# Optimization experiments

Hardware: AMD Instinct MI355X
Metric: run time of the kernel (lower is better)

## Reference

```python
import jax, jax.numpy as jnp
import numpy as np

B, T, E, H, NH, L, R, K, N, P, HOR = 32, 16, 768, 1024, 16, 6, 8, 16, 100000, 9, 8
HD = H // NH


def _ln(x, g, b):
    m = jnp.mean(x, -1, keepdims=True)
    v = jnp.mean((x - m) ** 2, -1, keepdims=True)
    return (x - m) * jax.lax.rsqrt(v + 1e-5) * g + b


def _lora(x, W, A, Bm, b):
    # base linear + low-rank update: x W^T + (x A^T) B^T + b
    return x @ W.T + (x @ A.T) @ Bm.T + b


def setup_inputs() -> dict:
    key = jax.random.key(0)
    ks = iter(jax.random.split(key, 64))
    def rn(shape, s):
        return jax.random.normal(next(ks), shape, dtype=jnp.float32) * s
    d = {}
    d['history_img_emb'] = rn((B, T, E), 1.0)
    d['current_emb'] = rn((B, E), 1.0)
    d['goal_emb'] = rn((B, E), 1.0)
    d['subgoal_emb'] = rn((B, E), 1.0)
    d['beacon_emb'] = rn((B, E), 1.0)
    d['history_proprio'] = rn((B, T, P), 1.0)
    d['proprio'] = rn((B, P), 1.0)
    d['bank'] = rn((N, E), 1.0)
    d['hp_W'] = rn((H, E + P), 0.02); d['hp_b'] = jnp.zeros((H,), jnp.float32)
    d['ip_W'] = rn((H, E), 0.02); d['ip_b'] = jnp.zeros((H,), jnp.float32)
    d['pp_W'] = rn((H, P), 0.02); d['pp_b'] = jnp.zeros((H,), jnp.float32)
    d['plan_token'] = rn((1, 1, H), 0.02)
    d['ln1_g'] = jnp.ones((L, H), jnp.float32); d['ln1_b'] = jnp.zeros((L, H), jnp.float32)
    d['ln2_g'] = jnp.ones((L, H), jnp.float32); d['ln2_b'] = jnp.zeros((L, H), jnp.float32)
    for nm, o, i in (('q', H, H), ('k', H, H), ('v', H, H), ('o', H, H), ('f1', 4 * H, H), ('f2', H, 4 * H)):
        d[nm + 'W'] = rn((L, o, i), 0.02)
        d[nm + 'A'] = rn((L, R, i), 0.02)
        d[nm + 'B'] = rn((L, o, R), 0.02)
        d[nm + 'b'] = jnp.zeros((L, o), jnp.float32)
    d['fln_g'] = jnp.ones((H,), jnp.float32); d['fln_b'] = jnp.zeros((H,), jnp.float32)
    d['ah_W1'] = rn((H, H), 0.02); d['ah_b1'] = jnp.zeros((H,), jnp.float32)
    d['ah_W2'] = rn((3, H), 0.02); d['ah_b2'] = jnp.zeros((3,), jnp.float32)
    d['rh_W1'] = rn((H, H + 3), 0.02); d['rh_b1'] = jnp.zeros((H,), jnp.float32)
    d['rh_W2'] = rn((HOR * 3, H), 0.02); d['rh_b2'] = jnp.zeros((HOR * 3,), jnp.float32)
    d['sh_W'] = rn((1, H), 0.02); d['sh_b'] = jnp.zeros((1,), jnp.float32)
    return d


def reference(history_img_emb, current_emb, goal_emb, subgoal_emb, beacon_emb,
              history_proprio, proprio, bank,
              hp_W, hp_b, ip_W, ip_b, pp_W, pp_b, plan_token,
              ln1_g, ln1_b, ln2_g, ln2_b,
              qW, qA, qB, qb, kW, kA, kB, kb, vW, vA, vB, vb, oW, oA, oB, ob,
              f1W, f1A, f1B, f1b, f2W, f2A, f2B, f2b,
              fln_g, fln_b, ah_W1, ah_b1, ah_W2, ah_b2,
              rh_W1, rh_b1, rh_W2, rh_b2, sh_W, sh_b):
    # batched semantic-bank top-k retrieval (replaces the per-sample python loop)
    sims = current_emb @ bank.T                      # [B, N]
    scores, idx = jax.lax.top_k(sims, K)             # [B, K]
    sem = bank[idx] * scores[..., None]              # [B, K, E] gather + scale

    # multi-modal token fusion
    hist = jnp.concatenate([history_img_emb, history_proprio], -1) @ hp_W.T + hp_b  # [B, T, H]
    img = lambda e: e @ ip_W.T + ip_b
    goal_t = img(goal_emb)[:, None]
    sub_t = img(subgoal_emb)[:, None]
    bea_t = img(beacon_emb)[:, None]
    sem_t = img(sem)                                 # [B, K, H]
    prop_t = (proprio @ pp_W.T + pp_b)[:, None]
    plan_t = jnp.broadcast_to(plan_token, (B, 1, H))
    x = jnp.concatenate([plan_t, hist, goal_t, sub_t, bea_t, sem_t, prop_t], 1)  # [B, S=37, H]

    scale = 1.0 / np.sqrt(HD).astype(np.float32)
    for l in range(L):
        h = _ln(x, ln1_g[l], ln1_b[l])
        q = _lora(h, qW[l], qA[l], qB[l], qb[l]).reshape(B, -1, NH, HD)
        k = _lora(h, kW[l], kA[l], kB[l], kb[l]).reshape(B, -1, NH, HD)
        v = _lora(h, vW[l], vA[l], vB[l], vb[l]).reshape(B, -1, NH, HD)
        attn = jax.nn.softmax(jnp.einsum('bshd,bthd->bhst', q, k) * scale, axis=-1)
        out = jnp.einsum('bhst,bthd->bshd', attn, v).reshape(B, -1, H)
        x = x + _lora(out, oW[l], oA[l], oB[l], ob[l])
        h2 = _ln(x, ln2_g[l], ln2_b[l])
        x = x + _lora(jax.nn.gelu(_lora(h2, f1W[l], f1A[l], f1B[l], f1b[l]), approximate=False),
                      f2W[l], f2A[l], f2B[l], f2b[l])

    x = _ln(x, fln_g, fln_b)
    ps = x[:, 0]                                     # plan token state [B, H]
    anchor = jax.nn.gelu(ps @ ah_W1.T + ah_b1, approximate=False) @ ah_W2.T + ah_b2  # [B, 3]
    ref_in = jnp.concatenate([ps, anchor], -1)
    waypoints = (jax.nn.gelu(ref_in @ rh_W1.T + rh_b1, approximate=False) @ rh_W2.T + rh_b2).reshape(B, HOR, 3)
    stop_logit = (ps @ sh_W.T + sh_b)[:, 0]          # [B]
    return anchor, waypoints, stop_logit
```

## Files before the change

### kernel.cpp

```cpp
#include <hip/hip_runtime.h>
#include <float.h>
#include <math.h>

#define NB 100000
#define SEQ 37
#define NTOK 1184
#define TKCH 16

typedef __attribute__((ext_vector_type(8))) short short8;
typedef __attribute__((ext_vector_type(4))) float floatx4;

__device__ __forceinline__ short f2bf(float f) {
  union { float f; unsigned u; } x; x.f = f;
  unsigned r = x.u + 0x7fff + ((x.u >> 16) & 1);
  return (short)(r >> 16);
}

__device__ __forceinline__ float gelu_f(float v) {
  return 0.5f * v * (1.f + erff(v * 0.70710678118654752f));
}

__global__ __launch_bounds__(256) void wconv_all(const float* __restrict__ qW,
                                                 const float* __restrict__ kW,
                                                 const float* __restrict__ vW,
                                                 const float* __restrict__ oW,
                                                 const float* __restrict__ f1W,
                                                 const float* __restrict__ f2W,
                                                 short* __restrict__ wb) {
  const int l = blockIdx.x / 1536;
  const int t = blockIdx.x - l * 1536;
  const float* src; int Kd; size_t doff; int np, kc;
  if (t < 512) {
    const int w = t >> 7, ti = t & 127;
    const float* base = (w == 0) ? qW : (w == 1) ? kW : (w == 2) ? vW : oW;
    src = base + (size_t)l * 1024 * 1024;
    Kd = 1024; np = ti >> 4; kc = ti & 15;
    doff = (size_t)w * 1048576 + ((size_t)np * 16 + kc) * 8192;
  } else if (t < 1024) {
    const int ti = t - 512;
    src = f1W + (size_t)l * 4096 * 1024;
    Kd = 1024; np = ti >> 4; kc = ti & 15;
    doff = (size_t)4 * 1048576 + ((size_t)np * 16 + kc) * 8192;
  } else {
    const int ti = t - 1024;
    src = f2W + (size_t)l * 1024 * 4096;
    Kd = 4096; np = ti >> 6; kc = ti & 63;
    doff = (size_t)8 * 1048576 + ((size_t)np * 64 + kc) * 8192;
  }
  short* dst = wb + (size_t)l * 12 * 1048576 + doff;
  const float* sp = src + (size_t)(np * 128) * Kd + kc * 64;
  const int tid = threadIdx.x;
#pragma unroll
  for (int q = 0; q < 4; ++q) {
    const int d = q * 256 + tid;
    const int row = d >> 3, slot = d & 7;
    const int ss = slot ^ (row & 7);
    const float* s = sp + (size_t)row * Kd + ss * 8;
    const float4 u0 = *(const float4*)s;
    const float4 u1 = *(const float4*)(s + 4);
    short8 v;
    v[0] = f2bf(u0.x); v[1] = f2bf(u0.y); v[2] = f2bf(u0.z); v[3] = f2bf(u0.w);
    v[4] = f2bf(u1.x); v[5] = f2bf(u1.y); v[6] = f2bf(u1.z); v[7] = f2bf(u1.w);
    *(short8*)(dst + (size_t)d * 8) = v;
  }
}

__global__ __launch_bounds__(256) void gemm_bt(const float* __restrict__ A, int lda,
                                               const short* __restrict__ WT, size_t wzstride,
                                               const float* __restrict__ b0,
                                               const float* __restrict__ b1,
                                               const float* __restrict__ b2,
                                               const float* __restrict__ LT,
                                               const float* __restrict__ B0,
                                               const float* __restrict__ B1,
                                               const float* __restrict__ B2,
                                               float* __restrict__ C, size_t czstride,
                                               int ldc, int M, int K,
                                               int acc_flag, int gelu_flag,
                                               int ksn, float* __restrict__ part) {
  __shared__ short Al[2][64 * 64];
  __shared__ short Wl[2][128 * 64];
  const int z = blockIdx.z;
  const int kidx = (ksn > 1) ? z : 0;
  const float* bias = (ksn > 1 || z == 0) ? b0 : (z == 1) ? b1 : b2;
  const float* Bz = (ksn > 1 || z == 0) ? B0 : (z == 1) ? B1 : B2;
  if (ksn == 1) C += (size_t)z * czstride;
  const int nkc_tot = K >> 6;
  const int nkc = nkc_tot / ksn;
  const short* wt = WT + (size_t)((ksn > 1) ? 0 : z) * wzstride +
                    ((size_t)blockIdx.y * nkc_tot + (size_t)kidx * nkc) * 8192;
  const int tid = threadIdx.x;
  const int wid = tid >> 6, lane = tid & 63;
  const int wr = wid >> 1, wc = wid & 1;
  const int bm = blockIdx.x * 64, bn = blockIdx.y * 128;
  const int arow = tid >> 2;
  const int s0 = (tid & 3) * 2;

  floatx4 acc[2][4];
#pragma unroll
  for (int i = 0; i < 2; ++i)
#pragma unroll
    for (int j = 0; j < 4; ++j)
#pragma unroll
      for (int r = 0; r < 4; ++r) acc[i][j][r] = 0.f;

  const int ga = bm + arow;
  const bool aok = ga < M;
  const float* ap = A + (size_t)ga * lda + (size_t)kidx * nkc * 64;
  const int aswz = arow & 7;

  float4 ar[4];
  short8 wreg[4];

#define LOAD_A(kc_)                                                        \
  {                                                                        \
    _Pragma("unroll") for (int j = 0; j < 2; ++j) {                        \
      const int slot = s0 + j;                                             \
      if (aok) {                                                           \
        ar[j * 2] = *(const float4*)(ap + (kc_)*64 + slot * 8);            \
        ar[j * 2 + 1] = *(const float4*)(ap + (kc_)*64 + slot * 8 + 4);    \
      } else {                                                             \
        ar[j * 2] = make_float4(0.f, 0.f, 0.f, 0.f);                      \
        ar[j * 2 + 1] = make_float4(0.f, 0.f, 0.f, 0.f);                  \
      }                                                                    \
    }                                                                      \
  }
#define LOAD_W(kc_)                                                        \
  {                                                                        \
    _Pragma("unroll") for (int it = 0; it < 4; ++it)                       \
        wreg[it] = *(const short8*)(wt + (size_t)(kc_)*8192 + (it * 256 + tid) * 8); \
  }
#define WRITE_A(buf_)                                                      \
  {                                                                        \
    _Pragma("unroll") for (int j = 0; j < 2; ++j) {                        \
      const int slot = s0 + j;                                             \
      short8 s;                                                            \
      s[0] = f2bf(ar[j * 2].x); s[1] = f2bf(ar[j * 2].y);                  \
      s[2] = f2bf(ar[j * 2].z); s[3] = f2bf(ar[j * 2].w);                  \
      s[4] = f2bf(ar[j * 2 + 1].x); s[5] = f2bf(ar[j * 2 + 1].y);          \
      s[6] = f2bf(ar[j * 2 + 1].z); s[7] = f2bf(ar[j * 2 + 1].w);          \
      *(short8*)&Al[buf_][arow * 64 + ((slot ^ aswz) << 3)] = s;           \
    }                                                                      \
  }
#define WRITE_W(buf_)                                                      \
  {                                                                        \
    _Pragma("unroll") for (int it = 0; it < 4; ++it)                       \
        *(short8*)&Wl[buf_][(it * 256 + tid) * 8] = wreg[it];              \
  }

  LOAD_W(0) LOAD_A(0)
  WRITE_A(0) WRITE_W(0)
  __syncthreads();

  for (int t = 0; t < nkc; ++t) {
    const int cur = t & 1, nxt = cur ^ 1;
    const bool more = (t + 1 < nkc);
    if (more) { LOAD_W(t + 1) LOAD_A(t + 1) }
#pragma unroll
    for (int ks = 0; ks < 2; ++ks) {
      short8 af[2], wf[4];
#pragma unroll
      for (int i = 0; i < 2; ++i) {
        const int row = wr * 32 + i * 16 + (lane & 15);
        const int sa = (ks * 4 + (lane >> 4)) ^ (row & 7);
        af[i] = *(const short8*)&Al[cur][row * 64 + sa * 8];
      }
#pragma unroll
      for (int j = 0; j < 4; ++j) {
        const int col = wc * 64 + j * 16 + (lane & 15);
        const int sw2 = (ks * 4 + (lane >> 4)) ^ (col & 7);
        wf[j] = *(const short8*)&Wl[cur][col * 64 + sw2 * 8];
      }
#pragma unroll
      for (int i = 0; i < 2; ++i)
#pragma unroll
        for (int j = 0; j < 4; ++j)
          acc[i][j] = __builtin_amdgcn_mfma_f32_16x16x32_bf16(af[i], wf[j], acc[i][j], 0, 0, 0);
    }
    if (more) { WRITE_A(nxt) WRITE_W(nxt) }
    __syncthreads();
  }
#undef LOAD_A
#undef LOAD_W
#undef WRITE_A
#undef WRITE_W

  if (ksn > 1) {
#pragma unroll
    for (int i = 0; i < 2; ++i) {
      const int gm0 = bm + wr * 32 + i * 16 + (lane >> 4) * 4;
#pragma unroll
      for (int r = 0; r < 4; ++r) {
        const int gm = gm0 + r;
        if (gm >= M) continue;
#pragma unroll
        for (int j = 0; j < 4; ++j) {
          const int gn = bn + wc * 64 + j * 16 + (lane & 15);
          part[((size_t)kidx * M + gm) * ldc + gn] = acc[i][j][r];
        }
      }
    }
    return;
  }

  float br[4][8];
  if (LT) {
#pragma unroll
    for (int j = 0; j < 4; ++j) {
      const int gn = bn + wc * 64 + j * 16 + (lane & 15);
      const float4 u0 = *(const float4*)(Bz + (size_t)gn * 8);
      const float4 u1 = *(const float4*)(Bz + (size_t)gn * 8 + 4);
      br[j][0] = u0.x; br[j][1] = u0.y; br[j][2] = u0.z; br[j][3] = u0.w;
      br[j][4] = u1.x; br[j][5] = u1.y; br[j][6] = u1.z; br[j][7] = u1.w;
    }
  }
#pragma unroll
  for (int i = 0; i < 2; ++i) {
    const int gm0 = bm + wr * 32 + i * 16 + (lane >> 4) * 4;
#pragma unroll
    for (int r = 0; r < 4; ++r) {
      const int gm = gm0 + r;
      if (gm >= M) continue;
      float lt[8];
      if (LT) {
        const float4 t0 = *(const float4*)(LT + ((size_t)z * NTOK + gm) * 8);
        const float4 t1 = *(const float4*)(LT + ((size_t)z * NTOK + gm) * 8 + 4);
        lt[0] = t0.x; lt[1] = t0.y; lt[2] = t0.z; lt[3] = t0.w;
        lt[4] = t1.x; lt[5] = t1.y; lt[6] = t1.z; lt[7] = t1.w;
      }
#pragma unroll
      for (int j = 0; j < 4; ++j) {
        const int gn = bn + wc * 64 + j * 16 + (lane & 15);
        float o = acc[i][j][r] + bias[gn];
        if (LT)
          o += lt[0] * br[j][0] + lt[1] * br[j][1] + lt[2] * br[j][2] + lt[3] * br[j][3] +
               lt[4] * br[j][4] + lt[5] * br[j][5] + lt[6] * br[j][6] + lt[7] * br[j][7];
        const size_t off = (size_t)gm * ldc + gn;
        if (acc_flag) o += C[off];
        if (gelu_flag) o = gelu_f(o);
        C[off] = o;
      }
    }
  }
}

__global__ __launch_bounds__(256) void reduce_f2(const float* __restrict__ part,
                                                 const float* __restrict__ bias,
                                                 const float* __restrict__ LT,
                                                 const float* __restrict__ Bm,
                                                 float* __restrict__ X) {
  const int idx = blockIdx.x * 256 + threadIdx.x;
  if (idx >= NTOK * 1024) return;
  const int gm = idx >> 10, gn = idx & 1023;
  float s = part[idx] + part[(size_t)NTOK * 1024 + idx] +
            part[(size_t)2 * NTOK * 1024 + idx] + part[(size_t)3 * NTOK * 1024 + idx];
  const float* t = LT + (size_t)gm * 8;
  const float* bp = Bm + (size_t)gn * 8;
  s += t[0] * bp[0] + t[1] * bp[1] + t[2] * bp[2] + t[3] * bp[3] +
       t[4] * bp[4] + t[5] * bp[5] + t[6] * bp[6] + t[7] * bp[7];
  X[idx] += s + bias[gn];
}

__global__ __launch_bounds__(256) void gemm_bf16(const float* __restrict__ A, int lda,
                                                 const float* __restrict__ W, int ldw,
                                                 const float* __restrict__ bias,
                                                 float* __restrict__ C,
                                                 int ldc, int M, int N, int K, int acc_flag) {
  __shared__ short Al[128 * 64];
  __shared__ short Wl[128 * 64];
  const int tid = threadIdx.x;
  const int wid = tid >> 6, lane = tid & 63;
  const int wr = wid >> 1, wc = wid & 1;
  const int bm = blockIdx.x * 128, bn = blockIdx.y * 128;
  const int srow = tid >> 1;
  const int sbase = (tid & 1) * 4;

  floatx4 acc[4][4];
#pragma unroll
  for (int i = 0; i < 4; ++i)
#pragma unroll
    for (int j = 0; j < 4; ++j)
#pragma unroll
      for (int r = 0; r < 4; ++r) acc[i][j][r] = 0.f;

  const int ga = bm + srow;
  const int gw = bn + srow;
  const bool aok = ga < M;
  const float* ap = A + (size_t)ga * lda;
  const float* wp = W + (size_t)gw * ldw;
  const int aswz = (srow & 7);
  const int dsbase = srow * 64;

  for (int kc = 0; kc < K; kc += 64) {
    __syncthreads();
    const bool kfull = (kc + 64 <= K);
    {
      const bool fast = aok && kfull && ((lda & 3) == 0);
#pragma unroll
      for (int j = 0; j < 4; ++j) {
        const int slot = sbase + j, k0 = slot * 8;
        float v[8];
        if (fast) {
          float4 u0 = *(const float4*)(ap + kc + k0);
          float4 u1 = *(const float4*)(ap + kc + k0 + 4);
          v[0] = u0.x; v[1] = u0.y; v[2] = u0.z; v[3] = u0.w;
          v[4] = u1.x; v[5] = u1.y; v[6] = u1.z; v[7] = u1.w;
        } else {
#pragma unroll
          for (int e = 0; e < 8; ++e) {
            int kk = kc + k0 + e;
            v[e] = (aok && kk < K) ? ap[kk] : 0.f;
          }
        }
        short8 s;
#pragma unroll
        for (int e = 0; e < 8; ++e) s[e] = f2bf(v[e]);
        *(short8*)&Al[dsbase + ((slot ^ aswz) << 3)] = s;
      }
    }
    {
      const bool fast = kfull && ((ldw & 3) == 0);
#pragma unroll
      for (int j = 0; j < 4; ++j) {
        const int slot = sbase + j, k0 = slot * 8;
        float v[8];
        if (fast) {
          float4 u0 = *(const float4*)(wp + kc + k0);
          float4 u1 = *(const float4*)(wp + kc + k0 + 4);
          v[0] = u0.x; v[1] = u0.y; v[2] = u0.z; v[3] = u0.w;
          v[4] = u1.x; v[5] = u1.y; v[6] = u1.z; v[7] = u1.w;
        } else {
#pragma unroll
          for (int e = 0; e < 8; ++e) {
            int kk = kc + k0 + e;
            v[e] = (kk < K) ? wp[kk] : 0.f;
          }
        }
        short8 s;
#pragma unroll
        for (int e = 0; e < 8; ++e) s[e] = f2bf(v[e]);
        *(short8*)&Wl[dsbase + ((slot ^ aswz) << 3)] = s;
      }
    }
    __syncthreads();
#pragma unroll
    for (int ks = 0; ks < 2; ++ks) {
      short8 af[4], wf[4];
#pragma unroll
      for (int i = 0; i < 4; ++i) {
        const int row = wr * 64 + i * 16 + (lane & 15);
        const int sa = (ks * 4 + (lane >> 4)) ^ (row & 7);
        af[i] = *(const short8*)&Al[row * 64 + sa * 8];
        const int col = wc * 64 + i * 16 + (lane & 15);
        const int sw = (ks * 4 + (lane >> 4)) ^ (col & 7);
        wf[i] = *(const short8*)&Wl[col * 64 + sw * 8];
      }
#pragma unroll
      for (int i = 0; i < 4; ++i)
#pragma unroll
        for (int j = 0; j < 4; ++j)
          acc[i][j] = __builtin_amdgcn_mfma_f32_16x16x32_bf16(af[i], wf[j], acc[i][j], 0, 0, 0);
    }
  }
#pragma unroll
  for (int i = 0; i < 4; ++i) {
    const int gm0 = bm + wr * 64 + i * 16 + (lane >> 4) * 4;
#pragma unroll
    for (int j = 0; j < 4; ++j) {
      const int gn = bn + wc * 64 + j * 16 + (lane & 15);
#pragma unroll
      for (int r = 0; r < 4; ++r) {
        const int gm = gm0 + r;
        if (gm < M) {
          float o = acc[i][j][r] + bias[gn];
          size_t off = (size_t)gm * ldc + gn;
          if (acc_flag) o += C[off];
          C[off] = o;
        }
      }
    }
  }
}

__global__ __launch_bounds__(256) void gemm_sm2(const float* __restrict__ A, int lda,
                                                const float* __restrict__ W, int ldw,
                                                const float* __restrict__ bias,
                                                float* __restrict__ C, int ldc,
                                                float* __restrict__ part,
                                                int N, int K, int gelu_flag) {
  __shared__ float buf[8192];
  const int tid = threadIdx.x;
  const int col = tid >> 3, ksub = tid & 7;
  const int gcol = blockIdx.x * 32 + col;
  const int KS = gridDim.y, ky = blockIdx.y;
  const int kchunk = (((K + KS - 1) / KS) + 127) & ~127;
  const int kstart = ky * kchunk;
  const int kend = (kstart + kchunk < K) ? (kstart + kchunk) : K;
  const float* wp = W + (size_t)(gcol < N ? gcol : 0) * ldw;

  float acc[32];
#pragma unroll
  for (int m = 0; m < 32; ++m) acc[m] = 0.f;

  for (int kc = kstart; kc < kend; kc += 128) {
    __syncthreads();
#pragma unroll
    for (int q = 0; q < 4; ++q) {
      const int idx4 = q * 256 + tid;
      const int m = idx4 >> 5, j = (idx4 & 31) * 4;
      const int gk = kc + j;
      float4 v;
      if (gk + 3 < K) {
        v = *(const float4*)(A + (size_t)m * lda + gk);
      } else {
        v.x = (gk < K) ? A[(size_t)m * lda + gk] : 0.f;
        v.y = (gk + 1 < K) ? A[(size_t)m * lda + gk + 1] : 0.f;
        v.z = (gk + 2 < K) ? A[(size_t)m * lda + gk + 2] : 0.f;
        v.w = (gk + 3 < K) ? A[(size_t)m * lda + gk + 3] : 0.f;
      }
      *(float4*)&buf[m * 128 + j] = v;
    }
    __syncthreads();
#pragma unroll
    for (int kk = 0; kk < 4; ++kk) {
      const int j = kk * 32 + ksub * 4;
      const int gk = kc + j;
      float4 w4 = make_float4(0.f, 0.f, 0.f, 0.f);
      if (gcol < N && gk < K) {
        if (gk + 3 < K) {
          w4 = *(const float4*)(wp + gk);
        } else {
          w4.x = wp[gk];
          if (gk + 1 < K) w4.y = wp[gk + 1];
          if (gk + 2 < K) w4.z = wp[gk + 2];
        }
      }
#pragma unroll
      for (int m = 0; m < 32; ++m) {
        const float4 a4 = *(const float4*)&buf[m * 128 + j];
        acc[m] += a4.x * w4.x + a4.y * w4.y + a4.z * w4.z + a4.w * w4.w;
      }
    }
  }
  __syncthreads();
#pragma unroll
  for (int m = 0; m < 32; ++m) buf[m * 256 + ksub * 32 + col] = acc[m];
  __syncthreads();
#pragma unroll
  for (int g = 0; g < 4; ++g) {
    const int idx = g * 256 + tid;
    const int m = idx >> 5, c = idx & 31;
    float s = 0.f;
#pragma unroll
    for (int h = 0; h < 8; ++h) s += buf[m * 256 + h * 32 + c];
    const int gc = blockIdx.x * 32 + c;
    if (gc < N) {
      if (KS == 1) {
        float o = s + bias[gc];
        if (gelu_flag) o = gelu_f(o);
        C[(size_t)m * ldc + gc] = o;
      } else {
        part[((size_t)ky * 32 + m) * N + gc] = s;
      }
    }
  }
}

__global__ __launch_bounds__(256) void reduce_sm(const float* __restrict__ part,
                                                 const float* __restrict__ bias,
                                                 float* __restrict__ C, int ldc,
                                                 int N, int KS, int gelu_flag) {
  const int idx = blockIdx.x * 256 + threadIdx.x;
  if (idx >= 32 * N) return;
  const int m = idx / N, c = idx - m * N;
  float s = 0.f;
  for (int h = 0; h < KS; ++h) s += part[((size_t)h * 32 + m) * N + c];
  float o = s + bias[c];
  if (gelu_flag) o = gelu_f(o);
  C[(size_t)m * ldc + c] = o;
}

__global__ __launch_bounds__(256) void sims_kernel(const float* __restrict__ cur,
                                                   const float* __restrict__ bank,
                                                   float* __restrict__ sims) {
  __shared__ float Bs[32][132];
  __shared__ float Cs[32][36];
  const int tid = threadIdx.x;
  const int tx = tid & 7;
  const int ty = tid >> 3;
  const int n0 = blockIdx.x * 128;
  const int srow = tid >> 1;
  const int spart = tid & 1;
  const int cb = tid >> 3;
  const int ck = (tid & 7) * 4;

  float acc[4][4] = {{0.f,0.f,0.f,0.f},{0.f,0.f,0.f,0.f},
                     {0.f,0.f,0.f,0.f},{0.f,0.f,0.f,0.f}};

  const bool rok = (n0 + srow) < NB;
  const float* bp = bank + (size_t)(n0 + srow) * 768 + spart * 16;
  const float* cp = cur + (size_t)cb * 768 + ck;

  for (int kc = 0; kc < 768; kc += 32) {
    __syncthreads();
#pragma unroll
    for (int jj = 0; jj < 4; ++jj) {
      float4 v = rok ? *(const float4*)(bp + kc + jj * 4)
                     : make_float4(0.f, 0.f, 0.f, 0.f);
      const int kk = spart * 16 + jj * 4;
      Bs[kk + 0][srow] = v.x; Bs[kk + 1][srow] = v.y;
      Bs[kk + 2][srow] = v.z; Bs[kk + 3][srow] = v.w;
    }
    {
      float4 v = *(const float4*)(cp + kc);
      Cs[ck + 0][cb] = v.x; Cs[ck + 1][cb] = v.y;
      Cs[ck + 2][cb] = v.z; Cs[ck + 3][cb] = v.w;
    }
    __syncthreads();
#pragma unroll
    for (int kk = 0; kk < 32; ++kk) {
      float4 av = *(const float4*)&Bs[kk][ty * 4];
      float4 bv = *(const float4*)&Cs[kk][tx * 4];
      float a4[4] = {av.x, av.y, av.z, av.w};
      float b4[4] = {bv.x, bv.y, bv.z, bv.w};
#pragma unroll
      for (int i = 0; i < 4; ++i)
#pragma unroll
        for (int j = 0; j < 4; ++j) acc[i][j] += a4[i] * b4[j];
    }
  }
  const int n = n0 + ty * 4;
#pragma unroll
  for (int j = 0; j < 4; ++j) {
    const int b = tx * 4 + j;
    float4 o = make_float4(acc[0][j], acc[1][j], acc[2][j], acc[3][j]);
    if (n + 3 < NB) {
      *(float4*)(sims + (size_t)b * NB + n) = o;
    } else {
      float oo[4] = {o.x, o.y, o.z, o.w};
      for (int i = 0; i < 4; ++i)
        if (n + i < NB) sims[(size_t)b * NB + n + i] = oo[i];
    }
  }
}

__global__ __launch_bounds__(256) void topk_stage1(const float* __restrict__ sims,
                                                   float* __restrict__ cv,
                                                   int* __restrict__ ci) {
  __shared__ float ss[4096];
  __shared__ int si[4096];
  __shared__ float wv[4];
  __shared__ int wi[4];
  const int chunk = blockIdx.x, b = blockIdx.y, tid = threadIdx.x;
  const int start = chunk * (NB / TKCH), end = start + (NB / TKCH);
  float ls[16]; int li[16];
#pragma unroll
  for (int i = 0; i < 16; ++i) { ls[i] = -FLT_MAX; li[i] = 0x7fffffff; }
  const float* row = sims + (size_t)b * NB;
  float lmin = -FLT_MAX;
  for (int n = start + tid; n < end; n += 256) {
    float v = row[n];
    if (v > lmin) {
      int p = 15;
      while (p > 0 && ls[p - 1] < v) { ls[p] = ls[p - 1]; li[p] = li[p - 1]; --p; }
      ls[p] = v; li[p] = n;
      lmin = ls[15];
    }
  }
#pragma unroll
  for (int i = 0; i < 16; ++i) { ss[i * 256 + tid] = ls[i]; si[i * 256 + tid] = li[i]; }
  __syncthreads();
  for (int round = 0; round < 16; ++round) {
    float bv = -FLT_MAX; int bi = 0x7fffffff;
#pragma unroll
    for (int i = 0; i < 16; ++i) {
      float v = ss[i * 256 + tid]; int ix = si[i * 256 + tid];
      if (v > bv || (v == bv && ix < bi)) { bv = v; bi = ix; }
    }
#pragma unroll
    for (int s = 32; s; s >>= 1) {
      float ov = __shfl_down(bv, s); int oi = __shfl_down(bi, s);
      if (ov > bv || (ov == bv && oi < bi)) { bv = ov; bi = oi; }
    }
    if ((tid & 63) == 0) { wv[tid >> 6] = bv; wi[tid >> 6] = bi; }
    __syncthreads();
    if (tid == 0) {
      bv = wv[0]; bi = wi[0];
      for (int w = 1; w < 4; ++w)
        if (wv[w] > bv || (wv[w] == bv && wi[w] < bi)) { bv = wv[w]; bi = wi[w]; }
      cv[(b * TKCH + chunk) * 16 + round] = bv;
      ci[(b * TKCH + chunk) * 16 + round] = bi;
      wi[0] = bi;
    }
    __syncthreads();
    bi = wi[0];
#pragma unroll
    for (int i = 0; i < 16; ++i)
      if (si[i * 256 + tid] == bi) ss[i * 256 + tid] = -FLT_MAX;
    __syncthreads();
  }
}

__global__ __launch_bounds__(256) void topk_stage2(const float* __restrict__ cv,
                                                   const int* __restrict__ ci,
                                                   float* __restrict__ tks,
                                                   int* __restrict__ tki) {
  __shared__ float wv[4];
  __shared__ int wi[4];
  __shared__ int bw;
  const int b = blockIdx.x, tid = threadIdx.x;
  float val = cv[b * 256 + tid];
  int idx = ci[b * 256 + tid];
  for (int round = 0; round < 16; ++round) {
    float bv = val; int bi = idx;
#pragma unroll
    for (int s = 1; s < 64; s <<= 1) {
      float ov = __shfl_xor(bv, s); int oi = __shfl_xor(bi, s);
      if (ov > bv || (ov == bv && oi < bi)) { bv = ov; bi = oi; }
    }
    if ((tid & 63) == 0) { wv[tid >> 6] = bv; wi[tid >> 6] = bi; }
    __syncthreads();
    if (tid == 0) {
      bv = wv[0]; bi = wi[0];
      for (int w = 1; w < 4; ++w)
        if (wv[w] > bv || (wv[w] == bv && wi[w] < bi)) { bv = wv[w]; bi = wi[w]; }
      tks[b * 16 + round] = bv; tki[b * 16 + round] = bi;
      bw = bi;
    }
    __syncthreads();
    if (idx == bw) val = -FLT_MAX;
  }
}

__global__ void sem_kernel(const float* __restrict__ bank, const float* __restrict__ tks,
                           const int* __restrict__ tki, float* __restrict__ sem) {
  int slot = blockIdx.x;
  float s = tks[slot]; int idx = tki[slot];
  for (int i = threadIdx.x; i < 768; i += 256)
    sem[(size_t)slot * 768 + i] = bank[(size_t)idx * 768 + i] * s;
}

__global__ void build_hist_in(const float* __restrict__ img, const float* __restrict__ pr,
                              float* __restrict__ out) {
  int r = blockIdx.x;
  for (int i = threadIdx.x; i < 777; i += 256)
    out[(size_t)r * 777 + i] = (i < 768) ? img[(size_t)r * 768 + i] : pr[r * 9 + (i - 768)];
}

__global__ void build_img_in(const float* __restrict__ goal, const float* __restrict__ sub,
                             const float* __restrict__ bea, const float* __restrict__ sem,
                             float* __restrict__ out) {
  int r = blockIdx.x;
  const float* src = (r < 32) ? goal + (size_t)r * 768
                   : (r < 64) ? sub + (size_t)(r - 32) * 768
                   : (r < 96) ? bea + (size_t)(r - 64) * 768
                              : sem + (size_t)(r - 96) * 768;
  for (int i = threadIdx.x; i < 768; i += 256) out[(size_t)r * 768 + i] = src[i];
}

__global__ void assemble_x(const float* __restrict__ th, const float* __restrict__ ti,
                           const float* __restrict__ tp, const float* __restrict__ plan,
                           float* __restrict__ x) {
  int r = blockIdx.x;
  int b = r / SEQ, tok = r - b * SEQ;
  const float* src;
  if (tok == 0) src = plan;
  else if (tok <= 16) src = th + (size_t)(b * 16 + tok - 1) * 1024;
  else if (tok <= 19) src = ti + (size_t)((tok - 17) * 32 + b) * 1024;
  else if (tok <= 35) src = ti + (size_t)(96 + b * 16 + (tok - 20)) * 1024;
  else src = tp + (size_t)b * 1024;
  for (int i = threadIdx.x; i < 1024; i += 256) x[(size_t)r * 1024 + i] = src[i];
}

__global__ void build_ref(const float* __restrict__ ps, const float* __restrict__ anc,
                          float* __restrict__ ref) {
  int b = blockIdx.x;
  for (int i = threadIdx.x; i < 1027; i += 256)
    ref[(size_t)b * 1027 + i] = (i < 1024) ? ps[(size_t)b * 1024 + i] : anc[b * 3 + (i - 1024)];
}

__device__ __forceinline__ float block_sum256(float v, float* red) {
#pragma unroll
  for (int s = 32; s; s >>= 1) v += __shfl_down(v, s);
  if ((threadIdx.x & 63) == 0) red[threadIdx.x >> 6] = v;
  __syncthreads();
  float tot = red[0] + red[1] + red[2] + red[3];
  __syncthreads();
  return tot;
}

__global__ __launch_bounds__(256) void ln_kernel(const float* __restrict__ in, int in_stride,
                                                 float* __restrict__ out,
                                                 const float* __restrict__ g,
                                                 const float* __restrict__ bt) {
  __shared__ float red[4];
  const float* xr = in + (size_t)blockIdx.x * in_stride;
  const int tid = threadIdx.x;
  float v[4];
#pragma unroll
  for (int i = 0; i < 4; ++i) v[i] = xr[tid + 256 * i];
  float mean = block_sum256(v[0] + v[1] + v[2] + v[3], red) * (1.f / 1024.f);
  float sq = 0.f;
#pragma unroll
  for (int i = 0; i < 4; ++i) { float d = v[i] - mean; sq += d * d; }
  float var = block_sum256(sq, red) * (1.f / 1024.f);
  float inv = rsqrtf(var + 1e-5f);
  float* orow = out + (size_t)blockIdx.x * 1024;
#pragma unroll
  for (int i = 0; i < 4; ++i) {
    int c = tid + 256 * i;
    orow[c] = (v[i] - mean) * inv * g[c] + bt[c];
  }
}

__global__ __launch_bounds__(256) void lora_down(const float* __restrict__ h,
                                                 const float* __restrict__ A0,
                                                 const float* __restrict__ A1,
                                                 const float* __restrict__ A2,
                                                 float* __restrict__ lt, int K) {
  __shared__ float red[4][8];
  const int m = blockIdx.x, z = blockIdx.y;
  const int tid = threadIdx.x, wave = tid >> 6, lane = tid & 63;
  const float* A = (z == 0) ? A0 : (z == 1) ? A1 : A2;
  float p[8] = {0.f, 0.f, 0.f, 0.f, 0.f, 0.f, 0.f, 0.f};
  for (int kk = tid; kk < K; kk += 256) {
    float hv = h[(size_t)m * K + kk];
#pragma unroll
    for (int r = 0; r < 8; ++r) p[r] += hv * A[r * K + kk];
  }
#pragma unroll
  for (int s = 1; s < 64; s <<= 1) {
#pragma unroll
    for (int r = 0; r < 8; ++r) p[r] += __shfl_xor(p[r], s);
  }
  if (lane == 0) {
#pragma unroll
    for (int r = 0; r < 8; ++r) red[wave][r] = p[r];
  }
  __syncthreads();
  if (tid < 8)
    lt[((size_t)z * NTOK + m) * 8 + tid] =
        red[0][tid] + red[1][tid] + red[2][tid] + red[3][tid];
}

__global__ __launch_bounds__(256) void attn_kernel(const float* __restrict__ q,
                                                   const float* __restrict__ k,
                                                   const float* __restrict__ v,
                                                   float* __restrict__ ao) {
  __shared__ float qs[SEQ * 64], ks[SEQ * 64], vs[SEQ * 64], sc[SEQ * 40];
  const int head = blockIdx.x, b = blockIdx.y, tid = threadIdx.x;
  const size_t base = ((size_t)b * SEQ) * 1024 + head * 64;
  for (int i = tid; i < SEQ * 64; i += 256) {
    int s = i >> 6, d = i & 63;
    size_t off = base + (size_t)s * 1024 + d;
    qs[i] = q[off]; ks[i] = k[off]; vs[i] = v[off];
  }
  __syncthreads();
  for (int p = tid; p < SEQ * SEQ; p += 256) {
    int s = p / SEQ, t = p - s * SEQ;
    float acc = 0.f;
#pragma unroll 16
    for (int d = 0; d < 64; ++d) acc += qs[s * 64 + d] * ks[t * 64 + d];
    sc[s * 40 + t] = acc * 0.125f;
  }
  __syncthreads();
  if (tid < SEQ) {
    float m = -FLT_MAX;
    for (int t = 0; t < SEQ; ++t) m = fmaxf(m, sc[tid * 40 + t]);
    float sum = 0.f;
    for (int t = 0; t < SEQ; ++t) { float e = expf(sc[tid * 40 + t] - m); sc[tid * 40 + t] = e; sum += e; }
    float inv = 1.f / sum;
    for (int t = 0; t < SEQ; ++t) sc[tid * 40 + t] *= inv;
  }
  __syncthreads();
  for (int i = tid; i < SEQ * 64; i += 256) {
    int s = i >> 6, d = i & 63;
    float acc = 0.f;
    for (int t = 0; t < SEQ; ++t) acc += sc[s * 40 + t] * vs[t * 64 + d];
    ao[base + (size_t)s * 1024 + d] = acc;
  }
}

extern "C" void kernel_launch(void* const* d_in, const int* in_sizes, int n_in,
                              void* d_out, int out_size, void* d_ws, size_t ws_size,
                              hipStream_t stream) {
  const float* hist_img = (const float*)d_in[0];
  const float* cur      = (const float*)d_in[1];
  const float* goal     = (const float*)d_in[2];
  const float* sub      = (const float*)d_in[3];
  const float* bea      = (const float*)d_in[4];
  const float* hist_pr  = (const float*)d_in[5];
  const float* prop     = (const float*)d_in[6];
  const float* bank     = (const float*)d_in[7];
  const float* hpW = (const float*)d_in[8];  const float* hpb = (const float*)d_in[9];
  const float* ipW = (const float*)d_in[10]; const float* ipb = (const float*)d_in[11];
  const float* ppW = (const float*)d_in[12]; const float* ppb = (const float*)d_in[13];
  const float* plan = (const float*)d_in[14];
  const float* ln1g = (const float*)d_in[15]; const float* ln1b = (const float*)d_in[16];
  const float* ln2g = (const float*)d_in[17]; const float* ln2b = (const float*)d_in[18];
  const float* qW = (const float*)d_in[19]; const float* qA = (const float*)d_in[20];
  const float* qB = (const float*)d_in[21]; const float* qb = (const float*)d_in[22];
  const float* kW = (const float*)d_in[23]; const float* kA = (const float*)d_in[24];
  const float* kB = (const float*)d_in[25]; const float* kb = (const float*)d_in[26];
  const float* vW = (const float*)d_in[27]; const float* vA = (const float*)d_in[28];
  const float* vB = (const float*)d_in[29]; const float* vb = (const float*)d_in[30];
  const float* oW = (const float*)d_in[31]; const float* oA = (const float*)d_in[32];
  const float* oB = (const float*)d_in[33]; const float* ob = (const float*)d_in[34];
  const float* f1W = (const float*)d_in[35]; const float* f1A = (const float*)d_in[36];
  const float* f1B = (const float*)d_in[37]; const float* f1b = (const float*)d_in[38];
  const float* f2W = (const float*)d_in[39]; const float* f2A = (const float*)d_in[40];
  const float* f2B = (const float*)d_in[41]; const float* f2b = (const float*)d_in[42];
  const float* flng = (const float*)d_in[43]; const float* flnb = (const float*)d_in[44];
  const float* ahW1 = (const float*)d_in[45]; const float* ahb1 = (const float*)d_in[46];
  const float* ahW2 = (const float*)d_in[47]; const float* ahb2 = (const float*)d_in[48];
  const float* rhW1 = (const float*)d_in[49]; const float* rhb1 = (const float*)d_in[50];
  const float* rhW2 = (const float*)d_in[51]; const float* rhb2 = (const float*)d_in[52];
  const float* shW = (const float*)d_in[53]; const float* shb = (const float*)d_in[54];
  float* out = (float*)d_out;

  float* ws  = (float*)d_ws;
  float* F1O = ws;
  float* SIMS = ws;
  float* X   = F1O + (size_t)NTOK * 4096;
  float* Hb  = X  + (size_t)NTOK * 1024;
  float* Qb  = Hb + (size_t)NTOK * 1024;
  float* Kb  = Qb + (size_t)NTOK * 1024;
  float* Vb  = Kb + (size_t)NTOK * 1024;
  float* AOb = Vb + (size_t)NTOK * 1024;
  float* LT  = AOb + (size_t)NTOK * 1024;
  float* SEM = LT + (size_t)3 * NTOK * 8;
  float* HIN = SEM + (size_t)512 * 768;
  float* TKS = HIN + (size_t)512 * 777;
  int*   TKI = (int*)(TKS + 512);
  float* PS  = TKS + 1024;
  float* HH  = PS + 32 * 1024;
  float* REF = HH + 32 * 1024;
  float* CV  = REF + 32 * 1027;
  int*   CI  = (int*)(CV + 32 * 256);
  float* PART = (float*)(CI + 32 * 256);
  float* PF2 = PART + 8 * 32 * 1024;
  short* WB  = (short*)(PF2 + (size_t)4 * NTOK * 1024);

  const size_t czs = (size_t)NTOK * 1024;
  const size_t WM = 1048576;
  const size_t WL = 12 * WM;

  auto gemmb1 = [&](const float* A, int lda, const float* W, int ldw, const float* bias,
                    float* C, int ldc, int M, int N, int K, int accf) {
    dim3 g((M + 127) / 128, N / 128, 1);
    gemm_bf16<<<g, 256, 0, stream>>>(A, lda, W, ldw, bias, C, ldc, M, N, K, accf);
  };
  auto gemms = [&](const float* A, int lda, const float* W, int ldw, const float* bias,
                   float* C, int ldc, int N, int K, int geluf, int KS) {
    gemm_sm2<<<dim3((N + 31) / 32, KS), 256, 0, stream>>>(A, lda, W, ldw, bias,
                                                          C, ldc, PART, N, K, geluf);
    if (KS > 1)
      reduce_sm<<<(32 * N + 255) / 256, 256, 0, stream>>>(PART, bias, C, ldc, N, KS, geluf);
  };

  wconv_all<<<6 * 1536, 256, 0, stream>>>(qW, kW, vW, oW, f1W, f2W, WB);

  sims_kernel<<<(NB + 127) / 128, 256, 0, stream>>>(cur, bank, SIMS);
  topk_stage1<<<dim3(TKCH, 32), 256, 0, stream>>>(SIMS, CV, CI);
  topk_stage2<<<32, 256, 0, stream>>>(CV, CI, TKS, TKI);
  sem_kernel<<<512, 256, 0, stream>>>(bank, TKS, TKI, SEM);

  build_hist_in<<<512, 256, 0, stream>>>(hist_img, hist_pr, HIN);
  build_img_in<<<608, 256, 0, stream>>>(goal, sub, bea, SEM, AOb);
  gemmb1(HIN, 777, hpW, 777, hpb, Qb, 1024, 512, 1024, 777, 0);
  gemmb1(AOb, 768, ipW, 768, ipb, Kb, 1024, 608, 1024, 768, 0);
  gemms(prop, 9, ppW, 9, ppb, Vb, 1024, 1024, 9, 0, 1);
  assemble_x<<<NTOK, 256, 0, stream>>>(Qb, Kb, Vb, plan, X);

  const int mblk = (NTOK + 63) / 64;
  for (int l = 0; l < 6; ++l) {
    const size_t aO = (size_t)l * 8 * 1024, bO = (size_t)l * 1024 * 8,
                 biO = (size_t)l * 1024;
    const size_t a4O = (size_t)l * 8 * 4096, b4O = (size_t)l * 4096 * 8,
                 bi4O = (size_t)l * 4096;
    const short* WBl = WB + (size_t)l * WL;
    ln_kernel<<<NTOK, 256, 0, stream>>>(X, 1024, Hb, ln1g + biO, ln1b + biO);
    lora_down<<<dim3(NTOK, 3), 256, 0, stream>>>(Hb, qA + aO, kA + aO, vA + aO, LT, 1024);
    gemm_bt<<<dim3(mblk, 8, 3), 256, 0, stream>>>(
        Hb, 1024, WBl, WM, qb + biO, kb + biO, vb + biO,
        LT, qB + bO, kB + bO, vB + bO, Qb, czs, 1024, NTOK, 1024, 0, 0, 1, nullptr);
    attn_kernel<<<dim3(16, 32), 256, 0, stream>>>(Qb, Kb, Vb, AOb);
    lora_down<<<dim3(NTOK, 1), 256, 0, stream>>>(AOb, oA + aO, oA + aO, oA + aO, LT, 1024);
    gemm_bt<<<dim3(mblk, 8, 1), 256, 0, stream>>>(
        AOb, 1024, WBl + 3 * WM, 0, ob + biO, ob + biO, ob + biO,
        LT, oB + bO, oB + bO, oB + bO, X, 0, 1024, NTOK, 1024, 1, 0, 1, nullptr);
    ln_kernel<<<NTOK, 256, 0, stream>>>(X, 1024, Hb, ln2g + biO, ln2b + biO);
    lora_down<<<dim3(NTOK, 1), 256, 0, stream>>>(Hb, f1A + aO, f1A + aO, f1A + aO, LT, 1024);
    gemm_bt<<<dim3(mblk, 32, 1), 256, 0, stream>>>(
        Hb, 1024, WBl + 4 * WM, 0, f1b + bi4O, f1b + bi4O, f1b + bi4O,
        LT, f1B + b4O, f1B + b4O, f1B + b4O, F1O, 0, 4096, NTOK, 1024, 0, 1, 1, nullptr);
    lora_down<<<dim3(NTOK, 1), 256, 0, stream>>>(F1O, f2A + a4O, f2A + a4O, f2A + a4O, LT, 4096);
    gemm_bt<<<dim3(mblk, 8, 4), 256, 0, stream>>>(
        F1O, 4096, WBl + 8 * WM, 0, f2b + biO, f2b + biO, f2b + biO,
        nullptr, nullptr, nullptr, nullptr, nullptr, 0, 1024, NTOK, 4096, 0, 0, 4, PF2);
    reduce_f2<<<(NTOK * 1024 + 255) / 256, 256, 0, stream>>>(PF2, f2b + biO, LT,
                                                             f2B + bO, X);
  }

  ln_kernel<<<32, 256, 0, stream>>>(X, SEQ * 1024, PS, flng, flnb);
  gemms(PS, 1024, ahW1, 1024, ahb1, HH, 1024, 1024, 1024, 1, 8);
  gemms(HH, 1024, ahW2, 1024, ahb2, out, 3, 3, 1024, 0, 8);
  build_ref<<<32, 256, 0, stream>>>(PS, out, REF);
  gemms(REF, 1027, rhW1, 1027, rhb1, HH, 1024, 1024, 1027, 1, 8);
  gemms(HH, 1024, rhW2, 1024, rhb2, out + 96, 24, 24, 1024, 0, 8);
  gemms(PS, 1024, shW, 1024, shb, out + 864, 1, 1, 1024, 0, 8);
}
```

Measured before the change: 1.908 ms.

## Route embedding GEMMs through pre-swizzled bf16 gemm_bt and split-K the o-projection

Hist and image projection weights are converted once into the swizzled bf16 layout, so the embedding GEMMs use gemm_bt instead of the generic fp32-loading gemm_bf16. The hist input is padded to K=832 so it tiles evenly. The o-projection now runs with split-K of 2 into partial buffers, followed by a generalized reduce kernel that adds the LoRA, bias and residual. This trades an extra conversion launch and an extra reduce pass for better GPU occupancy on the 1024x1024 o-proj and cheaper embedding GEMMs.

```diff
diff --git a/kernel.cpp b/kernel.cpp
--- a/kernel.cpp
+++ b/kernel.cpp
@@ -61,6 +61,30 @@
     short8 v;
     v[0] = f2bf(u0.x); v[1] = f2bf(u0.y); v[2] = f2bf(u0.z); v[3] = f2bf(u0.w);
     v[4] = f2bf(u1.x); v[5] = f2bf(u1.y); v[6] = f2bf(u1.z); v[7] = f2bf(u1.w);
+    *(short8*)(dst + (size_t)d * 8) = v;
+  }
+}
+
+__global__ __launch_bounds__(256) void wconv_embed(const float* __restrict__ hpW,
+                                                   const float* __restrict__ ipW,
+                                                   short* __restrict__ wbe) {
+  const int t = blockIdx.x;
+  const float* src; int Kd, np, kc; size_t doff;
+  if (t < 104) { src = hpW; Kd = 777; np = t / 13; kc = t - np * 13; doff = (size_t)t * 8192; }
+  else { const int ti = t - 104; src = ipW; Kd = 768; np = ti / 12; kc = ti - np * 12;
+         doff = (size_t)t * 8192; }
+  short* dst = wbe + doff;
+  const int tid = threadIdx.x;
+#pragma unroll
+  for (int q = 0; q < 4; ++q) {
+    const int d = q * 256 + tid;
+    const int row = d >> 3, slot = d & 7;
+    const int ss = slot ^ (row & 7);
+    const int gk0 = kc * 64 + ss * 8;
+    const float* s = src + (size_t)(np * 128 + row) * Kd;
+    short8 v;
+#pragma unroll
+    for (int e = 0; e < 8; ++e) v[e] = (gk0 + e < Kd) ? f2bf(s[gk0 + e]) : (short)0;
     *(short8*)(dst + (size_t)d * 8) = v;
   }
 }
@@ -244,142 +268,21 @@
   }
 }
 
-__global__ __launch_bounds__(256) void reduce_f2(const float* __restrict__ part,
+__global__ __launch_bounds__(256) void reduce_ks(const float* __restrict__ part,
                                                  const float* __restrict__ bias,
                                                  const float* __restrict__ LT,
                                                  const float* __restrict__ Bm,
-                                                 float* __restrict__ X) {
+                                                 float* __restrict__ X, int KS) {
   const int idx = blockIdx.x * 256 + threadIdx.x;
   if (idx >= NTOK * 1024) return;
   const int gm = idx >> 10, gn = idx & 1023;
-  float s = part[idx] + part[(size_t)NTOK * 1024 + idx] +
-            part[(size_t)2 * NTOK * 1024 + idx] + part[(size_t)3 * NTOK * 1024 + idx];
+  float s = 0.f;
+  for (int h = 0; h < KS; ++h) s += part[(size_t)h * NTOK * 1024 + idx];
   const float* t = LT + (size_t)gm * 8;
   const float* bp = Bm + (size_t)gn * 8;
   s += t[0] * bp[0] + t[1] * bp[1] + t[2] * bp[2] + t[3] * bp[3] +
        t[4] * bp[4] + t[5] * bp[5] + t[6] * bp[6] + t[7] * bp[7];
   X[idx] += s + bias[gn];
-}
-
-__global__ __launch_bounds__(256) void gemm_bf16(const float* __restrict__ A, int lda,
-                                                 const float* __restrict__ W, int ldw,
-                                                 const float* __restrict__ bias,
-                                                 float* __restrict__ C,
-                                                 int ldc, int M, int N, int K, int acc_flag) {
-  __shared__ short Al[128 * 64];
-  __shared__ short Wl[128 * 64];
-  const int tid = threadIdx.x;
-  const int wid = tid >> 6, lane = tid & 63;
-  const int wr = wid >> 1, wc = wid & 1;
-  const int bm = blockIdx.x * 128, bn = blockIdx.y * 128;
-  const int srow = tid >> 1;
-  const int sbase = (tid & 1) * 4;
-
-  floatx4 acc[4][4];
-#pragma unroll
-  for (int i = 0; i < 4; ++i)
-#pragma unroll
-    for (int j = 0; j < 4; ++j)
-#pragma unroll
-      for (int r = 0; r < 4; ++r) acc[i][j][r] = 0.f;
-
-  const int ga = bm + srow;
-  const int gw = bn + srow;
-  const bool aok = ga < M;
-  const float* ap = A + (size_t)ga * lda;
-  const float* wp = W + (size_t)gw * ldw;
-  const int aswz = (srow & 7);
-  const int dsbase = srow * 64;
-
-  for (int kc = 0; kc < K; kc += 64) {
-    __syncthreads();
-    const bool kfull = (kc + 64 <= K);
-    {
-      const bool fast = aok && kfull && ((lda & 3) == 0);
-#pragma unroll
-      for (int j = 0; j < 4; ++j) {
-        const int slot = sbase + j, k0 = slot * 8;
-        float v[8];
-        if (fast) {
-          float4 u0 = *(const float4*)(ap + kc + k0);
-          float4 u1 = *(const float4*)(ap + kc + k0 + 4);
-          v[0] = u0.x; v[1] = u0.y; v[2] = u0.z; v[3] = u0.w;
-          v[4] = u1.x; v[5] = u1.y; v[6] = u1.z; v[7] = u1.w;
-        } else {
-#pragma unroll
-          for (int e = 0; e < 8; ++e) {
-            int kk = kc + k0 + e;
-            v[e] = (aok && kk < K) ? ap[kk] : 0.f;
-          }
-        }
-        short8 s;
-#pragma unroll
-        for (int e = 0; e < 8; ++e) s[e] = f2bf(v[e]);
-        *(short8*)&Al[dsbase + ((slot ^ aswz) << 3)] = s;
-      }
-    }
-    {
-      const bool fast = kfull && ((ldw & 3) == 0);
-#pragma unroll
-      for (int j = 0; j < 4; ++j) {
-        const int slot = sbase + j, k0 = slot * 8;
-        float v[8];
-        if (fast) {
-          float4 u0 = *(const float4*)(wp + kc + k0);
-          float4 u1 = *(const float4*)(wp + kc + k0 + 4);
-          v[0] = u0.x; v[1] = u0.y; v[2] = u0.z; v[3] = u0.w;
-          v[4] = u1.x; v[5] = u1.y; v[6] = u1.z; v[7] = u1.w;
-        } else {
-#pragma unroll
-          for (int e = 0; e < 8; ++e) {
-            int kk = kc + k0 + e;
-            v[e] = (kk < K) ? wp[kk] : 0.f;
-          }
-        }
-        short8 s;
-#pragma unroll
-        for (int e = 0; e < 8; ++e) s[e] = f2bf(v[e]);
-        *(short8*)&Wl[dsbase + ((slot ^ aswz) << 3)] = s;
-      }
-    }
-    __syncthreads();
-#pragma unroll
-    for (int ks = 0; ks < 2; ++ks) {
-      short8 af[4], wf[4];
-#pragma unroll
-      for (int i = 0; i < 4; ++i) {
-        const int row = wr * 64 + i * 16 + (lane & 15);
-        const int sa = (ks * 4 + (lane >> 4)) ^ (row & 7);
-        af[i] = *(const short8*)&Al[row * 64 + sa * 8];
-        const int col = wc * 64 + i * 16 + (lane & 15);
-        const int sw = (ks * 4 + (lane >> 4)) ^ (col & 7);
-        wf[i] = *(const short8*)&Wl[col * 64 + sw * 8];
-      }
-#pragma unroll
-      for (int i = 0; i < 4; ++i)
-#pragma unroll
-        for (int j = 0; j < 4; ++j)
-          acc[i][j] = __builtin_amdgcn_mfma_f32_16x16x32_bf16(af[i], wf[j], acc[i][j], 0, 0, 0);
-    }
-  }
-#pragma unroll
-  for (int i = 0; i < 4; ++i) {
-    const int gm0 = bm + wr * 64 + i * 16 + (lane >> 4) * 4;
-#pragma unroll
-    for (int j = 0; j < 4; ++j) {
-      const int gn = bn + wc * 64 + j * 16 + (lane & 15);
-#pragma unroll
-      for (int r = 0; r < 4; ++r) {
-        const int gm = gm0 + r;
-        if (gm < M) {
-          float o = acc[i][j][r] + bias[gn];
-          size_t off = (size_t)gm * ldc + gn;
-          if (acc_flag) o += C[off];
-          C[off] = o;
-        }
-      }
-    }
-  }
 }
 
 __global__ __launch_bounds__(256) void gemm_sm2(const float* __restrict__ A, int lda,
@@ -643,8 +546,9 @@
 __global__ void build_hist_in(const float* __restrict__ img, const float* __restrict__ pr,
                               float* __restrict__ out) {
   int r = blockIdx.x;
-  for (int i = threadIdx.x; i < 777; i += 256)
-    out[(size_t)r * 777 + i] = (i < 768) ? img[(size_t)r * 768 + i] : pr[r * 9 + (i - 768)];
+  for (int i = threadIdx.x; i < 832; i += 256)
+    out[(size_t)r * 832 + i] = (i < 768) ? img[(size_t)r * 768 + i]
+                             : (i < 777) ? pr[r * 9 + (i - 768)] : 0.f;
 }
 
 __global__ void build_img_in(const float* __restrict__ goal, const float* __restrict__ sub,
@@ -830,7 +734,7 @@
   float* LT  = AOb + (size_t)NTOK * 1024;
   float* SEM = LT + (size_t)3 * NTOK * 8;
   float* HIN = SEM + (size_t)512 * 768;
-  float* TKS = HIN + (size_t)512 * 777;
+  float* TKS = HIN + (size_t)512 * 832;
   int*   TKI = (int*)(TKS + 512);
   float* PS  = TKS + 1024;
   float* HH  = PS + 32 * 1024;
@@ -840,16 +744,12 @@
   float* PART = (float*)(CI + 32 * 256);
   float* PF2 = PART + 8 * 32 * 1024;
   short* WB  = (short*)(PF2 + (size_t)4 * NTOK * 1024);
+  short* WBE = WB + (size_t)6 * 12 * 1048576;
 
   const size_t czs = (size_t)NTOK * 1024;
   const size_t WM = 1048576;
   const size_t WL = 12 * WM;
 
-  auto gemmb1 = [&](const float* A, int lda, const float* W, int ldw, const float* bias,
-                    float* C, int ldc, int M, int N, int K, int accf) {
-    dim3 g((M + 127) / 128, N / 128, 1);
-    gemm_bf16<<<g, 256, 0, stream>>>(A, lda, W, ldw, bias, C, ldc, M, N, K, accf);
-  };
   auto gemms = [&](const float* A, int lda, const float* W, int ldw, const float* bias,
                    float* C, int ldc, int N, int K, int geluf, int KS) {
     gemm_sm2<<<dim3((N + 31) / 32, KS), 256, 0, stream>>>(A, lda, W, ldw, bias,
@@ -859,6 +759,7 @@
   };
 
   wconv_all<<<6 * 1536, 256, 0, stream>>>(qW, kW, vW, oW, f1W, f2W, WB);
+  wconv_embed<<<200, 256, 0, stream>>>(hpW, ipW, WBE);
 
   sims_kernel<<<(NB + 127) / 128, 256, 0, stream>>>(cur, bank, SIMS);
   topk_stage1<<<dim3(TKCH, 32), 256, 0, stream>>>(SIMS, CV, CI);
@@ -867,8 +768,12 @@
 
   build_hist_in<<<512, 256, 0, stream>>>(hist_img, hist_pr, HIN);
   build_img_in<<<608, 256, 0, stream>>>(goal, sub, bea, SEM, AOb);
-  gemmb1(HIN, 777, hpW, 777, hpb, Qb, 1024, 512, 1024, 777, 0);
-  gemmb1(AOb, 768, ipW, 768, ipb, Kb, 1024, 608, 1024, 768, 0);
+  gemm_bt<<<dim3(8, 8, 1), 256, 0, stream>>>(
+      HIN, 832, WBE, 0, hpb, hpb, hpb,
+      nullptr, nullptr, nullptr, nullptr, Qb, 0, 1024, 512, 832, 0, 0, 1, nullptr);
+  gemm_bt<<<dim3(10, 8, 1), 256, 0, stream>>>(
+      AOb, 768, WBE + (size_t)104 * 8192, 0, ipb, ipb, ipb,
+      nullptr, nullptr, nullptr, nullptr, Kb, 0, 1024, 608, 768, 0, 0, 1, nullptr);
   gemms(prop, 9, ppW, 9, ppb, Vb, 1024, 1024, 9, 0, 1);
   assemble_x<<<NTOK, 256, 0, stream>>>(Qb, Kb, Vb, plan, X);
 
@@ -886,9 +791,11 @@
         LT, qB + bO, kB + bO, vB + bO, Qb, czs, 1024, NTOK, 1024, 0, 0, 1, nullptr);
     attn_kernel<<<dim3(16, 32), 256, 0, stream>>>(Qb, Kb, Vb, AOb);
     lora_down<<<dim3(NTOK, 1), 256, 0, stream>>>(AOb, oA + aO, oA + aO, oA + aO, LT, 1024);
-    gemm_bt<<<dim3(mblk, 8, 1), 256, 0, stream>>>(
+    gemm_bt<<<dim3(mblk, 8, 2), 256, 0, stream>>>(
         AOb, 1024, WBl + 3 * WM, 0, ob + biO, ob + biO, ob + biO,
-        LT, oB + bO, oB + bO, oB + bO, X, 0, 1024, NTOK, 1024, 1, 0, 1, nullptr);
+        nullptr, nullptr, nullptr, nullptr, nullptr, 0, 1024, NTOK, 1024, 0, 0, 2, PF2);
+    reduce_ks<<<(NTOK * 1024 + 255) / 256, 256, 0, stream>>>(PF2, ob + biO, LT,
+                                                             oB + bO, X, 2);
     ln_kernel<<<NTOK, 256, 0, stream>>>(X, 1024, Hb, ln2g + biO, ln2b + biO);
     lora_down<<<dim3(NTOK, 1), 256, 0, stream>>>(Hb, f1A + aO, f1A + aO, f1A + aO, LT, 1024);
     gemm_bt<<<dim3(mblk, 32, 1), 256, 0, stream>>>(
@@ -898,8 +805,8 @@
     gemm_bt<<<dim3(mblk, 8, 4), 256, 0, stream>>>(
         F1O, 4096, WBl + 8 * WM, 0, f2b + biO, f2b + biO, f2b + biO,
         nullptr, nullptr, nullptr, nullptr, nullptr, 0, 1024, NTOK, 4096, 0, 0, 4, PF2);
-    reduce_f2<<<(NTOK * 1024 + 255) / 256, 256, 0, stream>>>(PF2, f2b + biO, LT,
-                                                             f2B + bO, X);
+    reduce_ks<<<(NTOK * 1024 + 255) / 256, 256, 0, stream>>>(PF2, f2b + biO, LT,
+                                                             f2B + bO, X, 4);
   }
 
   ln_kernel<<<32, 256, 0, stream>>>(X, SEQ * 1024, PS, flng, flnb);
```

Result: faster. 1.725 ms (-9.6%).
